# Kernel optimization log

Hardware: AMD Instinct MI355X
Metric: run time of the kernel (lower is better)

Reference implementation:

```python
import jax, jax.numpy as jnp
import numpy as np

B, S = 16, 32768
LEVELS = (5, 20)
TIME_DIM = 8
NUM_FREQS = 6  # frequency xyz encoder: 3*(1+2*6)=39 dims
HID = 128
IN_DIM = 3 * (1 + 2 * NUM_FREQS) + 2 * TIME_DIM  # 55


def setup_inputs() -> dict:
    key = jax.random.key(0)
    ks = jax.random.split(key, 16)
    time = jax.random.uniform(ks[0], (B,), dtype=jnp.float32)
    xyz = jax.random.uniform(ks[1], (B, S, 3), dtype=jnp.float32) * 2.0 - 1.0  # in [-1,1]
    te0 = jax.random.normal(ks[2], (LEVELS[0] + 1, TIME_DIM), dtype=jnp.float32)
    te1 = jax.random.normal(ks[3], (LEVELS[1] + 1, TIME_DIM), dtype=jnp.float32)
    W0 = jax.random.normal(ks[4], (IN_DIM, HID), dtype=jnp.float32) * 0.05
    b0 = jnp.zeros((HID,), dtype=jnp.float32)
    W1 = jax.random.normal(ks[5], (HID, HID), dtype=jnp.float32) * 0.05
    b1 = jnp.zeros((HID,), dtype=jnp.float32)
    W2 = jax.random.normal(ks[6], (HID, HID), dtype=jnp.float32) * 0.05
    b2 = jnp.zeros((HID,), dtype=jnp.float32)
    Wout = jax.random.normal(ks[7], (HID, 1), dtype=jnp.float32) * 0.05
    bout = jnp.zeros((1,), dtype=jnp.float32)
    return {"time": time, "xyz": xyz, "te0": te0, "te1": te1,
            "W0": W0, "b0": b0, "W1": W1, "b1": b1, "W2": W2, "b2": b2,
            "Wout": Wout, "bout": bout}


def _time_encode(t, emb, L):
    # bucketize t into L uniform intervals on [0,1), lerp between bucket endpoints
    tL = t * L
    idx = jnp.clip(jnp.floor(tL).astype(jnp.int32), 0, L - 1)  # (B,)
    w = (idx + 1).astype(t.dtype) - tL                          # weight for lower endpoint
    lerped = w[:, None] * emb[idx] + (1.0 - w)[:, None] * emb[idx + 1]
    # t >= 1: use last embedding directly (torch fallback branch)
    return jnp.where((t >= 1.0)[:, None], emb[L][None, :], lerped)


def _xyz_encode(x):
    # frequency encoding, include_input, freqs 2^0..2^(NUM_FREQS-1)
    freqs = jnp.asarray(2.0 ** np.arange(NUM_FREQS), dtype=x.dtype)  # (F,)
    xp = x[:, None, :] * freqs[None, :, None]                         # (N, F, 3)
    n = x.shape[0]
    return jnp.concatenate([x, jnp.sin(xp).reshape(n, -1), jnp.cos(xp).reshape(n, -1)], axis=-1)


def reference(time, xyz, te0, te1, W0, b0, W1, b1, W2, b2, Wout, bout):
    s = xyz.shape[1]
    t_enc = jnp.concatenate([_time_encode(time, te0, LEVELS[0]),
                             _time_encode(time, te1, LEVELS[1])], axis=-1)  # (B, 16)
    t_enc = jnp.repeat(t_enc, s, axis=0)          # (B*S, 16)  'B d -> (B S) d'
    pts = (xyz.reshape(-1, 3) + 1.0) / 2.0        # (B*S, 3)
    x = jnp.concatenate([t_enc, _xyz_encode(pts)], axis=1)  # (B*S, 55)
    x = jax.nn.relu(x @ W0 + b0)
    x = jax.nn.relu(x @ W1 + b1)
    x = jax.nn.relu(x @ W2 + b2)
    return x @ Wout + bout  # (B*S, 1)
```

## Files before the change

kernel.cpp:

```cpp
#include <hip/hip_runtime.h>

typedef _Float16 f16;
typedef __attribute__((ext_vector_type(2))) __fp16 fp16x2;
typedef __attribute__((ext_vector_type(8))) _Float16 f16x8;
typedef __attribute__((ext_vector_type(4))) float f32x4;
typedef __attribute__((ext_vector_type(4))) unsigned int u32x4;

#define NPTS   (16 * 32768)
#define W0P_OFF 0
#define W1P_OFF (16 * 1024)
#define W2P_OFF (48 * 1024)
#define WOP_OFF (80 * 1024)
#define FRAGS_BYTES (84 * 1024)
#define TENC_OFF FRAGS_BYTES
#define WS_NEEDED (FRAGS_BYTES + 1024)
#define LDS_TOTAL (4 * 4096)

__global__ void pack_weights(const float* __restrict__ time, const float* __restrict__ te0,
                             const float* __restrict__ te1, const float* __restrict__ W0,
                             const float* __restrict__ W1, const float* __restrict__ W2,
                             const float* __restrict__ Wout, unsigned char* __restrict__ ws) {
  const int bi = blockIdx.x;
  const int l = threadIdx.x;
  const int g = l >> 4, r16 = l & 15;
  if (bi < 84) {
    const float* W; int obase, fi, kt, mt, kmax; bool natural, outcol;
    if (bi < 16)      { W = W0;   fi = bi;      mt = fi >> 1; kt = fi & 1; obase = W0P_OFF; kmax = 55;  natural = true;  outcol = false; }
    else if (bi < 48) { W = W1;   fi = bi - 16; mt = fi >> 2; kt = fi & 3; obase = W1P_OFF; kmax = 128; natural = false; outcol = false; }
    else if (bi < 80) { W = W2;   fi = bi - 48; mt = fi >> 2; kt = fi & 3; obase = W2P_OFF; kmax = 128; natural = false; outcol = false; }
    else              { W = Wout; fi = bi - 80; mt = 0;       kt = fi;     obase = WOP_OFF; kmax = 128; natural = false; outcol = true;  }
    const int m = mt * 16 + r16;
    f16 vals[8] __attribute__((aligned(16)));
#pragma unroll
    for (int j = 0; j < 8; ++j) {
      const int k = natural ? (kt * 32 + g * 8 + j)
                            : (kt * 32 + (j >> 2) * 16 + g * 4 + (j & 3));
      float v = 0.f;
      if (k < kmax) v = outcol ? ((m == 0) ? Wout[k] : 0.f) : W[k * 128 + m];
      vals[j] = (f16)v;
    }
    *(u32x4*)(ws + obase + (fi * 64 + l) * 16) = *(const u32x4*)vals;
  } else {
    const int idx = (bi - 84) * 64 + l;
    const int b = idx >> 4, d = idx & 15;
    const float t = time[b];
    const float* emb; int L, dd;
    if (d < 8) { emb = te0; L = 5;  dd = d; }
    else       { emb = te1; L = 20; dd = d - 8; }
    const float tL = t * (float)L;
    int i = (int)floorf(tL);
    i = i < 0 ? 0 : (i > L - 1 ? L - 1 : i);
    const float wlo = (float)(i + 1) - tL;
    float v = wlo * emb[i * 8 + dd] + (1.f - wlo) * emb[(i + 1) * 8 + dd];
    if (t >= 1.f) v = emb[L * 8 + dd];
    ((float*)(ws + TENC_OFF))[idx] = v;
  }
}

template <int KT>
__device__ __forceinline__ void layer_swapped(const unsigned char* __restrict__ wsrc,
                                              const float* __restrict__ bias,
                                              const f16x8 (&Bin)[KT][4], f16x8 (&Bout)[4][4],
                                              int lane) {
  const int g4 = (lane >> 4) * 4;
  f16x8 A0b[6], A1b[6];
  float4 ba, bb;
  f32x4 acc[2][4];
#pragma unroll
  for (int s = 0; s < 5; ++s) {
    const int mtp = s / KT, kt = s % KT;
    A0b[s] = *(const f16x8*)(wsrc + (((2 * mtp)     * KT + kt) * 64 + lane) * 16);
    A1b[s] = *(const f16x8*)(wsrc + (((2 * mtp + 1) * KT + kt) * 64 + lane) * 16);
  }
#pragma unroll
  for (int s = 0; s < 4 * KT; ++s) {
    const int mtp = s / KT, kt = s % KT, cb = s % 6;
    if (kt == 0) {
      ba = *(const float4*)(bias + mtp * 32 + g4);
      bb = *(const float4*)(bias + mtp * 32 + 16 + g4);
#pragma unroll
      for (int nt = 0; nt < 4; ++nt) {
        acc[0][nt] = (f32x4){0.f, 0.f, 0.f, 0.f};
        acc[1][nt] = (f32x4){0.f, 0.f, 0.f, 0.f};
      }
    }
    if (s + 5 < 4 * KT) {
      const int mtp2 = (s + 5) / KT, kt2 = (s + 5) % KT, pb = (s + 5) % 6;
      A0b[pb] = *(const f16x8*)(wsrc + (((2 * mtp2)     * KT + kt2) * 64 + lane) * 16);
      A1b[pb] = *(const f16x8*)(wsrc + (((2 * mtp2 + 1) * KT + kt2) * 64 + lane) * 16);
    }
    __builtin_amdgcn_s_setprio(1);
#pragma unroll
    for (int nt = 0; nt < 4; ++nt)
      acc[0][nt] = __builtin_amdgcn_mfma_f32_16x16x32_f16(A0b[cb], Bin[kt][nt], acc[0][nt], 0, 0, 0);
#pragma unroll
    for (int nt = 0; nt < 4; ++nt)
      acc[1][nt] = __builtin_amdgcn_mfma_f32_16x16x32_f16(A1b[cb], Bin[kt][nt], acc[1][nt], 0, 0, 0);
    __builtin_amdgcn_s_setprio(0);
    if (kt == KT - 1) {
      const float* bap = (const float*)&ba;
      const float* bbp = (const float*)&bb;
#pragma unroll
      for (int nt = 0; nt < 4; ++nt) {
        union { fp16x2 h2[4]; f16x8 v; } u;
        u.h2[0] = __builtin_amdgcn_cvt_pkrtz(fmaxf(acc[0][nt][0] + bap[0], 0.f), fmaxf(acc[0][nt][1] + bap[1], 0.f));
        u.h2[1] = __builtin_amdgcn_cvt_pkrtz(fmaxf(acc[0][nt][2] + bap[2], 0.f), fmaxf(acc[0][nt][3] + bap[3], 0.f));
        u.h2[2] = __builtin_amdgcn_cvt_pkrtz(fmaxf(acc[1][nt][0] + bbp[0], 0.f), fmaxf(acc[1][nt][1] + bbp[1], 0.f));
        u.h2[3] = __builtin_amdgcn_cvt_pkrtz(fmaxf(acc[1][nt][2] + bbp[2], 0.f), fmaxf(acc[1][nt][3] + bbp[3], 0.f));
        Bout[mtp][nt] = u.v;
      }
    }
  }
}

__global__ void __launch_bounds__(256, 2)
mlp_main(const float* __restrict__ xyz, const float* __restrict__ b0,
         const float* __restrict__ b1, const float* __restrict__ b2,
         const float* __restrict__ bout, const unsigned char* __restrict__ ws,
         float* __restrict__ out) {
  extern __shared__ char lds[];
  const int tid = threadIdx.x;
  const int lane = tid & 63, wv = tid >> 6;
  const int g = lane >> 4, r16 = lane & 15;

  char* scr = lds + wv * 4096;
  const float bo = bout[0];

  const int pbase = blockIdx.x * 256 + wv * 64;
  const int p = pbase + lane;

  f16 feat[64] __attribute__((aligned(16)));
  const float* tb = (const float*)(ws + TENC_OFF) + (blockIdx.x >> 7) * 16;
#pragma unroll
  for (int i = 0; i < 16; ++i) feat[i] = (f16)tb[i];
  const float xs0 = xyz[p * 3], xs1 = xyz[p * 3 + 1], xs2 = xyz[p * 3 + 2];
  const float pcs[3] = {(xs0 + 1.f) * 0.5f, (xs1 + 1.f) * 0.5f, (xs2 + 1.f) * 0.5f};
#pragma unroll
  for (int c = 0; c < 3; ++c) {
    feat[16 + c] = (f16)pcs[c];
    float s = __sinf(pcs[c]), co = __cosf(pcs[c]);
#pragma unroll
    for (int f = 0; f < 6; ++f) {
      feat[19 + f * 3 + c] = (f16)s;
      feat[37 + f * 3 + c] = (f16)co;
      const float s2 = 2.f * s * co, c2 = 1.f - 2.f * s * s;
      s = s2; co = c2;
    }
  }
#pragma unroll
  for (int i = 55; i < 64; ++i) feat[i] = (f16)0.f;

  f16x8 B0[2][4];
#pragma unroll
  for (int h = 0; h < 2; ++h) {
    if ((lane >> 5) == h) {
#pragma unroll
      for (int s = 0; s < 8; ++s)
        *(u32x4*)(scr + (lane & 31) * 128 + ((s ^ (lane & 7)) * 16)) = ((const u32x4*)feat)[s];
    }
    asm volatile("s_waitcnt lgkmcnt(0)" ::: "memory");
#pragma unroll
    for (int kt = 0; kt < 2; ++kt)
#pragma unroll
      for (int nn = 0; nn < 2; ++nn) {
        const int row = nn * 16 + r16;
        B0[kt][h * 2 + nn] = *(const f16x8*)(scr + row * 128 + (((4 * kt + g) ^ (row & 7)) * 16));
      }
    asm volatile("s_waitcnt lgkmcnt(0)" ::: "memory");
  }

  f16x8 Bx[4][4], By[4][4];
  layer_swapped<2>(ws + W0P_OFF, b0, B0, Bx, lane);
  layer_swapped<4>(ws + W1P_OFF, b1, Bx, By, lane);
  layer_swapped<4>(ws + W2P_OFF, b2, By, Bx, lane);

  f16x8 Ab[4];
#pragma unroll
  for (int kt = 0; kt < 4; ++kt)
    Ab[kt] = *(const f16x8*)(ws + WOP_OFF + (kt * 64 + lane) * 16);
  f32x4 accO[4];
#pragma unroll
  for (int nt = 0; nt < 4; ++nt) accO[nt] = (f32x4){bo, bo, bo, bo};
  __builtin_amdgcn_s_setprio(1);
#pragma unroll
  for (int kt = 0; kt < 4; ++kt) {
#pragma unroll
    for (int nt = 0; nt < 4; ++nt)
      accO[nt] = __builtin_amdgcn_mfma_f32_16x16x32_f16(Ab[kt], Bx[kt][nt], accO[nt], 0, 0, 0);
  }
  __builtin_amdgcn_s_setprio(0);

  const float a0 = __shfl(accO[0][0], r16, 64);
  const float a1 = __shfl(accO[1][0], r16, 64);
  const float a2 = __shfl(accO[2][0], r16, 64);
  const float a3 = __shfl(accO[3][0], r16, 64);
  const float v = g == 0 ? a0 : g == 1 ? a1 : g == 2 ? a2 : a3;
  out[pbase + lane] = v;
}

extern "C" void kernel_launch(void* const* d_in, const int* in_sizes, int n_in,
                              void* d_out, int out_size, void* d_ws, size_t ws_size,
                              hipStream_t stream) {
  const float* time = (const float*)d_in[0];
  const float* xyz  = (const float*)d_in[1];
  const float* te0  = (const float*)d_in[2];
  const float* te1  = (const float*)d_in[3];
  const float* W0   = (const float*)d_in[4];
  const float* b0   = (const float*)d_in[5];
  const float* W1   = (const float*)d_in[6];
  const float* b1   = (const float*)d_in[7];
  const float* W2   = (const float*)d_in[8];
  const float* b2   = (const float*)d_in[9];
  const float* Wout = (const float*)d_in[10];
  const float* bout = (const float*)d_in[11];
  float* out = (float*)d_out;
  unsigned char* ws = (unsigned char*)d_ws;
  if (ws_size < WS_NEEDED) return;

  pack_weights<<<88, 64, 0, stream>>>(time, te0, te1, W0, W1, W2, Wout, ws);
  mlp_main<<<NPTS / 256, 256, LDS_TOTAL, stream>>>(xyz, b0, b1, b2, bout, ws, out);
}
```

Measured before the change: 49.71 us.

## Fold bias into MFMA init, double-buffer accumulators, shrink weight prefetch ring

Each layer now loads all bias vectors up front and passes them as the initial accumulator of the first MFMA, which removes the separate bias adds in the epilogue. Accumulators are double-buffered by output tile parity so the ReLU/convert epilogue of one tile can overlap the next tile's MFMAs. The weight prefetch ring shrinks from depth 6 to depth 3 to save registers. Feature encoding is now computed in fp32 and packed into fp16 pairs with cvt_pkrtz instead of scalar fp16 stores. The output layer also seeds its accumulator with the output bias through the first MFMA.

Measured after the change: 49.79 us. About the same (+0.1%).

```diff
diff --git a/kernel.cpp b/kernel.cpp
--- a/kernel.cpp
+++ b/kernel.cpp
@@ -63,52 +63,57 @@
                                               const f16x8 (&Bin)[KT][4], f16x8 (&Bout)[4][4],
                                               int lane) {
   const int g4 = (lane >> 4) * 4;
-  f16x8 A0b[6], A1b[6];
-  float4 ba, bb;
-  f32x4 acc[2][4];
-#pragma unroll
-  for (int s = 0; s < 5; ++s) {
+  f16x8 A0b[3], A1b[3];
+  f32x4 bv[4][2];
+#pragma unroll
+  for (int mtp = 0; mtp < 4; ++mtp) {
+    bv[mtp][0] = *(const f32x4*)(bias + mtp * 32 + g4);
+    bv[mtp][1] = *(const f32x4*)(bias + mtp * 32 + 16 + g4);
+  }
+#pragma unroll
+  for (int s = 0; s < 2; ++s) {
     const int mtp = s / KT, kt = s % KT;
     A0b[s] = *(const f16x8*)(wsrc + (((2 * mtp)     * KT + kt) * 64 + lane) * 16);
     A1b[s] = *(const f16x8*)(wsrc + (((2 * mtp + 1) * KT + kt) * 64 + lane) * 16);
   }
-#pragma unroll
-  for (int s = 0; s < 4 * KT; ++s) {
-    const int mtp = s / KT, kt = s % KT, cb = s % 6;
-    if (kt == 0) {
-      ba = *(const float4*)(bias + mtp * 32 + g4);
-      bb = *(const float4*)(bias + mtp * 32 + 16 + g4);
-#pragma unroll
-      for (int nt = 0; nt < 4; ++nt) {
-        acc[0][nt] = (f32x4){0.f, 0.f, 0.f, 0.f};
-        acc[1][nt] = (f32x4){0.f, 0.f, 0.f, 0.f};
+  f32x4 acc[2][2][4];
+#pragma unroll
+  for (int mtp = 0; mtp < 4; ++mtp) {
+    const int par = mtp & 1;
+#pragma unroll
+    for (int kt = 0; kt < KT; ++kt) {
+      const int s = mtp * KT + kt, cb = s % 3;
+      if (s + 2 < 4 * KT) {
+        const int mtp2 = (s + 2) / KT, kt2 = (s + 2) % KT, pb = (s + 2) % 3;
+        A0b[pb] = *(const f16x8*)(wsrc + (((2 * mtp2)     * KT + kt2) * 64 + lane) * 16);
+        A1b[pb] = *(const f16x8*)(wsrc + (((2 * mtp2 + 1) * KT + kt2) * 64 + lane) * 16);
       }
-    }
-    if (s + 5 < 4 * KT) {
-      const int mtp2 = (s + 5) / KT, kt2 = (s + 5) % KT, pb = (s + 5) % 6;
-      A0b[pb] = *(const f16x8*)(wsrc + (((2 * mtp2)     * KT + kt2) * 64 + lane) * 16);
-      A1b[pb] = *(const f16x8*)(wsrc + (((2 * mtp2 + 1) * KT + kt2) * 64 + lane) * 16);
-    }
-    __builtin_amdgcn_s_setprio(1);
-#pragma unroll
-    for (int nt = 0; nt < 4; ++nt)
-      acc[0][nt] = __builtin_amdgcn_mfma_f32_16x16x32_f16(A0b[cb], Bin[kt][nt], acc[0][nt], 0, 0, 0);
-#pragma unroll
-    for (int nt = 0; nt < 4; ++nt)
-      acc[1][nt] = __builtin_amdgcn_mfma_f32_16x16x32_f16(A1b[cb], Bin[kt][nt], acc[1][nt], 0, 0, 0);
-    __builtin_amdgcn_s_setprio(0);
-    if (kt == KT - 1) {
-      const float* bap = (const float*)&ba;
-      const float* bbp = (const float*)&bb;
-#pragma unroll
-      for (int nt = 0; nt < 4; ++nt) {
-        union { fp16x2 h2[4]; f16x8 v; } u;
-        u.h2[0] = __builtin_amdgcn_cvt_pkrtz(fmaxf(acc[0][nt][0] + bap[0], 0.f), fmaxf(acc[0][nt][1] + bap[1], 0.f));
-        u.h2[1] = __builtin_amdgcn_cvt_pkrtz(fmaxf(acc[0][nt][2] + bap[2], 0.f), fmaxf(acc[0][nt][3] + bap[3], 0.f));
-        u.h2[2] = __builtin_amdgcn_cvt_pkrtz(fmaxf(acc[1][nt][0] + bbp[0], 0.f), fmaxf(acc[1][nt][1] + bbp[1], 0.f));
-        u.h2[3] = __builtin_amdgcn_cvt_pkrtz(fmaxf(acc[1][nt][2] + bbp[2], 0.f), fmaxf(acc[1][nt][3] + bbp[3], 0.f));
-        Bout[mtp][nt] = u.v;
+      __builtin_amdgcn_s_setprio(1);
+      if (kt == 0) {
+#pragma unroll
+        for (int nt = 0; nt < 4; ++nt)
+          acc[par][0][nt] = __builtin_amdgcn_mfma_f32_16x16x32_f16(A0b[cb], Bin[0][nt], bv[mtp][0], 0, 0, 0);
+#pragma unroll
+        for (int nt = 0; nt < 4; ++nt)
+          acc[par][1][nt] = __builtin_amdgcn_mfma_f32_16x16x32_f16(A1b[cb], Bin[0][nt], bv[mtp][1], 0, 0, 0);
+      } else {
+#pragma unroll
+        for (int nt = 0; nt < 4; ++nt)
+          acc[par][0][nt] = __builtin_amdgcn_mfma_f32_16x16x32_f16(A0b[cb], Bin[kt][nt], acc[par][0][nt], 0, 0, 0);
+#pragma unroll
+        for (int nt = 0; nt < 4; ++nt)
+          acc[par][1][nt] = __builtin_amdgcn_mfma_f32_16x16x32_f16(A1b[cb], Bin[kt][nt], acc[par][1][nt], 0, 0, 0);
       }
+      __builtin_amdgcn_s_setprio(0);
+    }
+#pragma unroll
+    for (int nt = 0; nt < 4; ++nt) {
+      union { fp16x2 h2[4]; f16x8 v; } u;
+      u.h2[0] = __builtin_amdgcn_cvt_pkrtz(fmaxf(acc[par][0][nt][0], 0.f), fmaxf(acc[par][0][nt][1], 0.f));
+      u.h2[1] = __builtin_amdgcn_cvt_pkrtz(fmaxf(acc[par][0][nt][2], 0.f), fmaxf(acc[par][0][nt][3], 0.f));
+      u.h2[2] = __builtin_amdgcn_cvt_pkrtz(fmaxf(acc[par][1][nt][0], 0.f), fmaxf(acc[par][1][nt][1], 0.f));
+      u.h2[3] = __builtin_amdgcn_cvt_pkrtz(fmaxf(acc[par][1][nt][2], 0.f), fmaxf(acc[par][1][nt][3], 0.f));
+      Bout[mtp][nt] = u.v;
     }
   }
 }
@@ -129,26 +134,33 @@
   const int pbase = blockIdx.x * 256 + wv * 64;
   const int p = pbase + lane;
 
-  f16 feat[64] __attribute__((aligned(16)));
+  float ff[64];
   const float* tb = (const float*)(ws + TENC_OFF) + (blockIdx.x >> 7) * 16;
 #pragma unroll
-  for (int i = 0; i < 16; ++i) feat[i] = (f16)tb[i];
+  for (int i = 0; i < 16; ++i) ff[i] = tb[i];
   const float xs0 = xyz[p * 3], xs1 = xyz[p * 3 + 1], xs2 = xyz[p * 3 + 2];
   const float pcs[3] = {(xs0 + 1.f) * 0.5f, (xs1 + 1.f) * 0.5f, (xs2 + 1.f) * 0.5f};
 #pragma unroll
   for (int c = 0; c < 3; ++c) {
-    feat[16 + c] = (f16)pcs[c];
+    ff[16 + c] = pcs[c];
     float s = __sinf(pcs[c]), co = __cosf(pcs[c]);
 #pragma unroll
     for (int f = 0; f < 6; ++f) {
-      feat[19 + f * 3 + c] = (f16)s;
-      feat[37 + f * 3 + c] = (f16)co;
+      ff[19 + f * 3 + c] = s;
+      ff[37 + f * 3 + c] = co;
       const float s2 = 2.f * s * co, c2 = 1.f - 2.f * s * s;
       s = s2; co = c2;
     }
   }
 #pragma unroll
-  for (int i = 55; i < 64; ++i) feat[i] = (f16)0.f;
+  for (int i = 55; i < 64; ++i) ff[i] = 0.f;
+  unsigned int fw[32];
+#pragma unroll
+  for (int i = 0; i < 32; ++i) {
+    union { fp16x2 h; unsigned int u; } cv;
+    cv.h = __builtin_amdgcn_cvt_pkrtz(ff[2 * i], ff[2 * i + 1]);
+    fw[i] = cv.u;
+  }
 
   f16x8 B0[2][4];
 #pragma unroll
@@ -156,7 +168,7 @@
     if ((lane >> 5) == h) {
 #pragma unroll
       for (int s = 0; s < 8; ++s)
-        *(u32x4*)(scr + (lane & 31) * 128 + ((s ^ (lane & 7)) * 16)) = ((const u32x4*)feat)[s];
+        *(u32x4*)(scr + (lane & 31) * 128 + ((s ^ (lane & 7)) * 16)) = ((const u32x4*)fw)[s];
     }
     asm volatile("s_waitcnt lgkmcnt(0)" ::: "memory");
 #pragma unroll
@@ -178,12 +190,14 @@
 #pragma unroll
   for (int kt = 0; kt < 4; ++kt)
     Ab[kt] = *(const f16x8*)(ws + WOP_OFF + (kt * 64 + lane) * 16);
+  const f32x4 bovec = (f32x4){bo, bo, bo, bo};
   f32x4 accO[4];
-#pragma unroll
-  for (int nt = 0; nt < 4; ++nt) accO[nt] = (f32x4){bo, bo, bo, bo};
   __builtin_amdgcn_s_setprio(1);
 #pragma unroll
-  for (int kt = 0; kt < 4; ++kt) {
+  for (int nt = 0; nt < 4; ++nt)
+    accO[nt] = __builtin_amdgcn_mfma_f32_16x16x32_f16(Ab[0], Bx[0][nt], bovec, 0, 0, 0);
+#pragma unroll
+  for (int kt = 1; kt < 4; ++kt) {
 #pragma unroll
     for (int nt = 0; nt < 4; ++nt)
       accO[nt] = __builtin_amdgcn_mfma_f32_16x16x32_f16(Ab[kt], Bx[kt][nt], accO[nt], 0, 0, 0);
```
